# Optimization experiments

Hardware: AMD Instinct MI355X
Metric: run time of the kernel (lower is better)

Reference implementation:

```python
import jax, jax.numpy as jnp
import numpy as np

INF = jnp.float32(1e10)  # stands in for +inf; squared dists here are < 3*256^2 so min is exact


def _dt1d(f, axis, block=16):
    """Exact 1D squared-Euclidean min-plus transform along `axis`:
    out[i] = min_j ( (i-j)^2 + f[j] ). Chunked over output positions to bound memory."""
    f = jnp.moveaxis(f, axis, -1)
    L = f.shape[-1]
    b = min(block, L)
    pad = (-L) % b
    ii = jnp.arange(L + pad).reshape(-1, b)  # output index blocks
    j = jnp.arange(L)

    def body(ib):  # ib: [b] output indices
        cost = ((ib[:, None] - j[None, :]) ** 2).astype(f.dtype)  # [b, L]
        return jnp.min(f[..., None, :] + cost, axis=-1)            # [..., b]

    out = jax.lax.map(body, ii)                 # [nb, ..., b]
    out = jnp.moveaxis(out, 0, -2)              # [..., nb, b]
    out = out.reshape(*f.shape[:-1], -1)[..., :L]
    return jnp.moveaxis(out, -1, axis)


def _edt(mask, axes):
    """Exact Euclidean distance transform: for voxels where mask is True,
    distance to the nearest voxel where mask is False (matches scipy distance_transform_edt)."""
    f = jnp.where(mask, INF, jnp.float32(0.0))  # squared distance init
    for ax in axes:  # separable exact EDT (Felzenszwalb decomposition via min-plus)
        f = _dt1d(f, ax)
    return jnp.sqrt(f)


def setup_inputs() -> dict:
    key = jax.random.key(0)
    k1, k2 = jax.random.split(key)
    N, C, H, W = 16, 4, 256, 256
    pred = jax.random.normal(k1, (N, C, H, W), dtype=jnp.float32)
    target = jax.random.randint(k2, (N, C, H, W), 0, 2, dtype=jnp.int32)
    return {"pred": pred, "target": target}


def reference(pred, target):
    # softmax over class dim
    p = jax.nn.softmax(pred, axis=1)
    # scipy EDT was applied per-sample on target[i] (a 3D [C,H,W] volume) of (target==0);
    # vectorized over the batch by transforming only axes (1,2,3).
    dist = _edt(target == 0, axes=(1, 2, 3))  # [N,C,H,W] float32
    return (p * dist).sum() / (dist.sum() + 1e-10)
```

## Files before the change

kernel.cpp:

```cpp
#include <hip/hip_runtime.h>
#include <math.h>

#define NS 16
#define HH 256
#define WW 256
#define PIX_PER_N 65536
#define CPLANE PIX_PER_N
#define SAMPLE_STRIDE (4*PIX_PER_N)
#define NPIX (NS*PIX_PER_N)

#define RWIN 8
#define T2 81
#define FLAG_CAP 4096
#define NWBLK (NS*64)


__device__ inline unsigned cpack(int x0, int x1, int x2, int x3) {
    int f0 = x0 ? 0 : 255;
    int f1 = x1 ? 0 : 255;
    int f2 = x2 ? 0 : 255;
    int f3 = x3 ? 0 : 255;
    int a0 = min(min(f0,     f1 + 1), min(f2 + 4, f3 + 9));
    int a1 = min(min(f0 + 1, f1    ), min(f2 + 1, f3 + 4));
    int a2 = min(min(f0 + 4, f1 + 1), min(f2,     f3 + 1));
    int a3 = min(min(f0 + 9, f1 + 4), min(f2 + 1, f3    ));
    return (unsigned)a0 | ((unsigned)a1 << 8) | ((unsigned)a2 << 16) | ((unsigned)a3 << 24);
}

__global__ __launch_bounds__(256) void k_cpass(const int4* __restrict__ tgt,
                                               uint4* __restrict__ A) {
    int i = blockIdx.x * 256 + threadIdx.x;
    int n = i >> 14;
    int q = i & 16383;
    const int4* base = tgt + n * 65536 + q;
    int4 t0 = base[0];
    int4 t1 = base[16384];
    int4 t2 = base[32768];
    int4 t3 = base[49152];
    uint4 r;
    r.x = cpack(t0.x, t1.x, t2.x, t3.x);
    r.y = cpack(t0.y, t1.y, t2.y, t3.y);
    r.z = cpack(t0.z, t1.z, t2.z, t3.z);
    r.w = cpack(t0.w, t1.w, t2.w, t3.w);
    A[i] = r;
}

__global__ __launch_bounds__(256) void k_hpass(const unsigned* __restrict__ A,
                                               unsigned* __restrict__ B) {
    int bid = blockIdx.x;
    int n = bid >> 6, b = bid & 63;
    int c = threadIdx.x;
    const unsigned* An = A + (n << 16) + c;
    unsigned ring[20];
    int h0 = b * 4 - RWIN;
#pragma unroll
    for (int k = 0; k < 20; ++k) {
        int h = h0 + k;
        ring[k] = ((unsigned)h < 256u) ? An[h << 8] : 0xFFFFFFFFu;
    }
    unsigned* Bn = B + (n << 16) + c;
#pragma unroll
    for (int i = 0; i < 4; ++i) {
        int v0 = 1023, v1 = 1023, v2 = 1023, v3 = 1023;
#pragma unroll
        for (int j = 0; j < 17; ++j) {
            unsigned x = ring[i + j];
            int cc = (j - 8) * (j - 8);
            v0 = min(v0, (int)(x & 255u) + cc);
            v1 = min(v1, (int)((x >> 8) & 255u) + cc);
            v2 = min(v2, (int)((x >> 16) & 255u) + cc);
            v3 = min(v3, (int)(x >> 24) + cc);
        }
        v0 = min(v0, 255); v1 = min(v1, 255); v2 = min(v2, 255); v3 = min(v3, 255);
        Bn[(b * 4 + i) << 8] = (unsigned)v0 | ((unsigned)v1 << 8) |
                               ((unsigned)v2 << 16) | ((unsigned)v3 << 24);
    }
}

__global__ __launch_bounds__(256) void k_wpass(const unsigned* __restrict__ B,
                                               const float* __restrict__ pred,
                                               double* __restrict__ partials,
                                               int* __restrict__ counter,
                                               int* __restrict__ list) {
    __shared__ unsigned rows[4][WW + 2 * RWIN];
    __shared__ double wred[8];

    int bid = blockIdx.x;
    int n = bid >> 6, b = bid & 63;
    int h0 = b * 4;
    int tid = threadIdx.x;
    const unsigned* Bn = B + (n << 16);

#pragma unroll
    for (int r = 0; r < 4; ++r)
        rows[r][RWIN + tid] = Bn[((h0 + r) << 8) + tid];
    if (tid < RWIN) {
#pragma unroll
        for (int r = 0; r < 4; ++r) {
            rows[r][tid] = 0xFFFFFFFFu;
            rows[r][WW + RWIN + tid] = 0xFFFFFFFFu;
        }
    }
    __syncthreads();

    float accp = 0.0f, accd = 0.0f;
#pragma unroll
    for (int r = 0; r < 4; ++r) {
        int v0 = 1023, v1 = 1023, v2 = 1023, v3 = 1023;
#pragma unroll
        for (int j = 0; j < 17; ++j) {
            unsigned x = rows[r][tid + j];
            int cc = (j - 8) * (j - 8);
            v0 = min(v0, (int)(x & 255u) + cc);
            v1 = min(v1, (int)((x >> 8) & 255u) + cc);
            v2 = min(v2, (int)((x >> 16) & 255u) + cc);
            v3 = min(v3, (int)(x >> 24) + cc);
        }
        int vv[4] = {v0, v1, v2, v3};
        float d[4];
        int gh = h0 + r;
#pragma unroll
        for (int c4 = 0; c4 < 4; ++c4) {
            if (vv[c4] >= T2) {
                int slot = atomicAdd(counter, 1);
                if (slot < FLAG_CAP) list[slot] = (((n << 2) | c4) << 16) | (gh << 8) | tid;
                d[c4] = 0.0f;
            } else {
                d[c4] = sqrtf((float)vv[c4]);
            }
        }
        const float* P = pred + n * SAMPLE_STRIDE + (gh << 8) + tid;
        float p0 = P[0], p1 = P[CPLANE], p2 = P[2 * CPLANE], p3 = P[3 * CPLANE];
        float m = fmaxf(fmaxf(p0, p1), fmaxf(p2, p3));
        float e0 = expf(p0 - m), e1 = expf(p1 - m), e2 = expf(p2 - m), e3 = expf(p3 - m);
        float inv = 1.0f / (e0 + e1 + e2 + e3);
        accp += (e0 * d[0] + e1 * d[1] + e2 * d[2] + e3 * d[3]) * inv;
        accd += d[0] + d[1] + d[2] + d[3];
    }

#pragma unroll
    for (int off = 32; off; off >>= 1) {
        accp += __shfl_down(accp, off, 64);
        accd += __shfl_down(accd, off, 64);
    }
    int lane = tid & 63, wv = tid >> 6;
    if (lane == 0) { wred[wv] = (double)accp; wred[4 + wv] = (double)accd; }
    __syncthreads();
    if (tid == 0) {
        partials[2 * bid]     = wred[0] + wred[1] + wred[2] + wred[3];
        partials[2 * bid + 1] = wred[4] + wred[5] + wred[6] + wred[7];
    }
}

__global__ __launch_bounds__(256) void k_final(const double* __restrict__ partials,
                                               const unsigned* __restrict__ gA,
                                               const float* __restrict__ pred,
                                               const int* __restrict__ counter,
                                               const int* __restrict__ list,
                                               float* __restrict__ out) {
    __shared__ double wred[8];
    __shared__ int red[4];
    __shared__ double fb[2];
    int tid = threadIdx.x;
    if (tid == 0) { fb[0] = 0.0; fb[1] = 0.0; }
    __syncthreads();

    int cnt = *counter;
    if (cnt > FLAG_CAP) cnt = FLAG_CAP;
    for (int i = 0; i < cnt; ++i) {
        int id = list[i];
        int nc = id >> 16;
        int nn = nc >> 2, c4 = nc & 3;
        int hh = (id >> 8) & 255, w = id & 255;
        int best = 0x7FFFFFFF;
        for (int p = tid; p < PIX_PER_N; p += 256) {
            unsigned x = gA[nn * PIX_PER_N + p];
            int ac = (int)((x >> (8 * c4)) & 255u);
            if (ac < 255) {
                int dh = (p >> 8) - hh, dw = (p & 255) - w;
                best = min(best, dh * dh + dw * dw + ac);
            }
        }
#pragma unroll
        for (int off = 32; off; off >>= 1) best = min(best, __shfl_down(best, off, 64));
        if ((tid & 63) == 0) red[tid >> 6] = best;
        __syncthreads();
        if (tid == 0) {
            int b = min(min(red[0], red[1]), min(red[2], red[3]));
            float d2 = (b == 0x7FFFFFFF) ? 1e10f : (float)b;
            float dist = sqrtf(d2);
            const float* PP = pred + nn * SAMPLE_STRIDE + (hh << 8) + w;
            float q0 = PP[0], q1 = PP[CPLANE], q2 = PP[2 * CPLANE], q3 = PP[3 * CPLANE];
            float mm = fmaxf(fmaxf(q0, q1), fmaxf(q2, q3));
            float g0 = expf(q0 - mm), g1 = expf(q1 - mm), g2 = expf(q2 - mm), g3 = expf(q3 - mm);
            float ginv = 1.0f / (g0 + g1 + g2 + g3);
            float pc = (c4 == 0 ? g0 : c4 == 1 ? g1 : c4 == 2 ? g2 : g3) * ginv;
            fb[0] += (double)(pc * dist);
            fb[1] += (double)dist;
        }
        __syncthreads();
    }

    double p = 0.0, d = 0.0;
    for (int i = tid; i < NWBLK; i += 256) {
        p += partials[2 * i];
        d += partials[2 * i + 1];
    }
#pragma unroll
    for (int off = 32; off; off >>= 1) {
        p += __shfl_down(p, off, 64);
        d += __shfl_down(d, off, 64);
    }
    int lane = tid & 63, wv = tid >> 6;
    if (lane == 0) { wred[wv] = p; wred[4 + wv] = d; }
    __syncthreads();
    if (tid == 0) {
        double pt = wred[0] + wred[1] + wred[2] + wred[3] + fb[0];
        double dt = wred[4] + wred[5] + wred[6] + wred[7] + fb[1];
        out[0] = (float)(pt / (dt + 1e-10));
    }
}

extern "C" void kernel_launch(void* const* d_in, const int* in_sizes, int n_in,
                              void* d_out, int out_size, void* d_ws, size_t ws_size,
                              hipStream_t stream) {
    const float* pred   = (const float*)d_in[0];
    const int*   target = (const int*)d_in[1];
    float* out = (float*)d_out;
    char* ws = (char*)d_ws;

    int*      counter  = (int*)ws;
    int*      list     = (int*)(ws + 64);
    double*   partials = (double*)(ws + 32768);
    unsigned* A        = (unsigned*)(ws + 131072);
    unsigned* B        = (unsigned*)(ws + 131072 + 4u * NPIX);

    hipMemsetAsync(ws, 0, 4, stream);
    k_cpass<<<NPIX / 1024, 256, 0, stream>>>((const int4*)target, (uint4*)A);
    k_hpass<<<NS * 64,     256, 0, stream>>>(A, B);
    k_wpass<<<NWBLK,       256, 0, stream>>>(B, pred, partials, counter, list);
    k_final<<<1,           256, 0, stream>>>(partials, A, pred, counter, list, out);
}
```

Baseline: 94.26 us.

## Fuse H and W min-plus passes, use packed 16-bit min, drop memset

Merges the column (H) pass into the row (W) kernel. Each block computes its 4 rows of H-transformed values into shared memory instead of writing an intermediate buffer B to global memory and reading it back. The min-plus inner loops now operate on two 16-bit lanes per 32-bit word with a packed min, which halves the instruction count. The counter reset moves from a separate memset into the first kernel. Together these remove one launch, one memset and a full-size global round trip, at the cost of more registers and shared memory per block.

```diff
diff --git a/kernel.cpp b/kernel.cpp
--- a/kernel.cpp
+++ b/kernel.cpp
@@ -14,6 +14,21 @@
 #define FLAG_CAP 4096
 #define NWBLK (NS*64)
 
+
+typedef unsigned short u16x2 __attribute__((ext_vector_type(2)));
+union PK { unsigned u; u16x2 v; };
+
+__device__ inline unsigned pkmin(unsigned a, unsigned b) {
+    PK x, y, r;
+    x.u = a; y.u = b;
+#if __has_builtin(__builtin_elementwise_min)
+    r.v = __builtin_elementwise_min(x.v, y.v);
+#else
+    r.v.x = x.v.x < y.v.x ? x.v.x : y.v.x;
+    r.v.y = x.v.y < y.v.y ? x.v.y : y.v.y;
+#endif
+    return r.u;
+}
 
 __device__ inline unsigned cpack(int x0, int x1, int x2, int x3) {
     int f0 = x0 ? 0 : 255;
@@ -28,8 +43,10 @@
 }
 
 __global__ __launch_bounds__(256) void k_cpass(const int4* __restrict__ tgt,
-                                               uint4* __restrict__ A) {
+                                               uint4* __restrict__ A,
+                                               int* __restrict__ counter) {
     int i = blockIdx.x * 256 + threadIdx.x;
+    if (i == 0) *counter = 0;
     int n = i >> 14;
     int q = i & 16383;
     const int4* base = tgt + n * 65536 + q;
@@ -45,60 +62,45 @@
     A[i] = r;
 }
 
-__global__ __launch_bounds__(256) void k_hpass(const unsigned* __restrict__ A,
-                                               unsigned* __restrict__ B) {
-    int bid = blockIdx.x;
-    int n = bid >> 6, b = bid & 63;
-    int c = threadIdx.x;
-    const unsigned* An = A + (n << 16) + c;
-    unsigned ring[20];
-    int h0 = b * 4 - RWIN;
-#pragma unroll
-    for (int k = 0; k < 20; ++k) {
-        int h = h0 + k;
-        ring[k] = ((unsigned)h < 256u) ? An[h << 8] : 0xFFFFFFFFu;
-    }
-    unsigned* Bn = B + (n << 16) + c;
-#pragma unroll
-    for (int i = 0; i < 4; ++i) {
-        int v0 = 1023, v1 = 1023, v2 = 1023, v3 = 1023;
-#pragma unroll
-        for (int j = 0; j < 17; ++j) {
-            unsigned x = ring[i + j];
-            int cc = (j - 8) * (j - 8);
-            v0 = min(v0, (int)(x & 255u) + cc);
-            v1 = min(v1, (int)((x >> 8) & 255u) + cc);
-            v2 = min(v2, (int)((x >> 16) & 255u) + cc);
-            v3 = min(v3, (int)(x >> 24) + cc);
-        }
-        v0 = min(v0, 255); v1 = min(v1, 255); v2 = min(v2, 255); v3 = min(v3, 255);
-        Bn[(b * 4 + i) << 8] = (unsigned)v0 | ((unsigned)v1 << 8) |
-                               ((unsigned)v2 << 16) | ((unsigned)v3 << 24);
-    }
-}
-
-__global__ __launch_bounds__(256) void k_wpass(const unsigned* __restrict__ B,
-                                               const float* __restrict__ pred,
-                                               double* __restrict__ partials,
-                                               int* __restrict__ counter,
-                                               int* __restrict__ list) {
-    __shared__ unsigned rows[4][WW + 2 * RWIN];
+__global__ __launch_bounds__(256) void k_hw(const unsigned* __restrict__ A,
+                                            const float* __restrict__ pred,
+                                            double* __restrict__ partials,
+                                            int* __restrict__ counter,
+                                            int* __restrict__ list) {
+    __shared__ uint2 sB[4][WW + 16];
     __shared__ double wred[8];
 
     int bid = blockIdx.x;
     int n = bid >> 6, b = bid & 63;
     int h0 = b * 4;
     int tid = threadIdx.x;
-    const unsigned* Bn = B + (n << 16);
-
-#pragma unroll
-    for (int r = 0; r < 4; ++r)
-        rows[r][RWIN + tid] = Bn[((h0 + r) << 8) + tid];
+
+    const unsigned* An = A + (n << 16) + tid;
+    uint2 ring[20];
+#pragma unroll
+    for (int k = 0; k < 20; ++k) {
+        int h = h0 - RWIN + k;
+        unsigned x = ((unsigned)h < 256u) ? An[h << 8] : 0xFFFFFFFFu;
+        ring[k].x = x & 0x00FF00FFu;
+        ring[k].y = (x >> 8) & 0x00FF00FFu;
+    }
+
+#pragma unroll
+    for (int r = 0; r < 4; ++r) {
+        unsigned vlo = 0x03FF03FFu, vhi = 0x03FF03FFu;
+#pragma unroll
+        for (int j = 0; j < 17; ++j) {
+            unsigned a = (unsigned)((j - 8) * (j - 8)) * 0x00010001u;
+            vlo = pkmin(vlo, ring[r + j].x + a);
+            vhi = pkmin(vhi, ring[r + j].y + a);
+        }
+        sB[r][RWIN + tid] = make_uint2(vlo, vhi);
+    }
     if (tid < RWIN) {
 #pragma unroll
         for (int r = 0; r < 4; ++r) {
-            rows[r][tid] = 0xFFFFFFFFu;
-            rows[r][WW + RWIN + tid] = 0xFFFFFFFFu;
+            sB[r][tid]            = make_uint2(0x03FF03FFu, 0x03FF03FFu);
+            sB[r][WW + RWIN + tid] = make_uint2(0x03FF03FFu, 0x03FF03FFu);
         }
     }
     __syncthreads();
@@ -106,19 +108,21 @@
     float accp = 0.0f, accd = 0.0f;
 #pragma unroll
     for (int r = 0; r < 4; ++r) {
-        int v0 = 1023, v1 = 1023, v2 = 1023, v3 = 1023;
+        unsigned vlo = 0x03FF03FFu, vhi = 0x03FF03FFu;
 #pragma unroll
         for (int j = 0; j < 17; ++j) {
-            unsigned x = rows[r][tid + j];
-            int cc = (j - 8) * (j - 8);
-            v0 = min(v0, (int)(x & 255u) + cc);
-            v1 = min(v1, (int)((x >> 8) & 255u) + cc);
-            v2 = min(v2, (int)((x >> 16) & 255u) + cc);
-            v3 = min(v3, (int)(x >> 24) + cc);
-        }
-        int vv[4] = {v0, v1, v2, v3};
+            uint2 x = sB[r][tid + j];
+            unsigned a = (unsigned)((j - 8) * (j - 8)) * 0x00010001u;
+            vlo = pkmin(vlo, x.x + a);
+            vhi = pkmin(vhi, x.y + a);
+        }
+        int vv[4];
+        vv[0] = (int)(vlo & 0xFFFFu);
+        vv[2] = (int)(vlo >> 16);
+        vv[1] = (int)(vhi & 0xFFFFu);
+        vv[3] = (int)(vhi >> 16);
+        int gh = h0 + r;
         float d[4];
-        int gh = h0 + r;
 #pragma unroll
         for (int c4 = 0; c4 < 4; ++c4) {
             if (vv[c4] >= T2) {
@@ -233,11 +237,8 @@
     int*      list     = (int*)(ws + 64);
     double*   partials = (double*)(ws + 32768);
     unsigned* A        = (unsigned*)(ws + 131072);
-    unsigned* B        = (unsigned*)(ws + 131072 + 4u * NPIX);
-
-    hipMemsetAsync(ws, 0, 4, stream);
-    k_cpass<<<NPIX / 1024, 256, 0, stream>>>((const int4*)target, (uint4*)A);
-    k_hpass<<<NS * 64,     256, 0, stream>>>(A, B);
-    k_wpass<<<NWBLK,       256, 0, stream>>>(B, pred, partials, counter, list);
+
+    k_cpass<<<NPIX / 1024, 256, 0, stream>>>((const int4*)target, (uint4*)A, counter);
+    k_hw   <<<NWBLK,       256, 0, stream>>>(A, pred, partials, counter, list);
     k_final<<<1,           256, 0, stream>>>(partials, A, pred, counter, list, out);
 }
```

Measured after the change: 87.51 us. 7.2% less time.
